# Kernel tuning notes

Measured on AMD Instinct MI355X. Metric: run time of the kernel, lower is better.

## Reference

```python
import jax, jax.numpy as jnp
import numpy as np

NUM_HEADS = 8
NUM_GROUPS = 32
EPS = 1e-5


def setup_inputs() -> dict:
    key = jax.random.key(0)
    ks = jax.random.split(key, 12)
    B, C, H, W = 8, 512, 32, 32
    E = 512
    s = 1.0 / np.sqrt(C)
    inp = {
        "input_tensor": jax.random.normal(ks[0], (B, C, H, W), dtype=jnp.float32),
        "Wq": jax.random.normal(ks[1], (C, E), dtype=jnp.float32) * s,
        "bq": jnp.zeros((E,), dtype=jnp.float32),
        "Wk": jax.random.normal(ks[2], (C, E), dtype=jnp.float32) * s,
        "bk": jnp.zeros((E,), dtype=jnp.float32),
        "Wv": jax.random.normal(ks[3], (C, E), dtype=jnp.float32) * s,
        "bv": jnp.zeros((E,), dtype=jnp.float32),
        "Wo": jax.random.normal(ks[4], (E, E), dtype=jnp.float32) * s,
        "bo": jnp.zeros((E,), dtype=jnp.float32),
        "gamma": jnp.ones((E,), dtype=jnp.float32),
        "beta": jnp.zeros((E,), dtype=jnp.float32),
    }
    return inp


def reference(input_tensor, Wq, bq, Wk, bk, Wv, bv, Wo, bo, gamma, beta):
    B, C, H, W = input_tensor.shape
    E = Wq.shape[1]
    nH = NUM_HEADS
    hd = E // nH
    S = H * W

    # [B, C, H, W] -> [B, S, C]
    x = input_tensor.reshape(B, C, S).transpose(0, 2, 1)

    q = (x @ Wq + bq).reshape(B, S, nH, hd).transpose(0, 2, 1, 3)  # [B, h, S, d]
    k = (x @ Wk + bk).reshape(B, S, nH, hd).transpose(0, 2, 1, 3)
    v = (x @ Wv + bv).reshape(B, S, nH, hd).transpose(0, 2, 1, 3)

    scale = hd ** (-0.5)
    scores = jnp.einsum("bhqd,bhkd->bhqk", q, k) * scale
    weights = jax.nn.softmax(scores, axis=-1)
    attn = jnp.einsum("bhqk,bhkd->bhqd", weights, v)  # [B, h, S, d]

    attn = attn.transpose(0, 2, 1, 3).reshape(B, S, E)
    out = attn @ Wo + bo  # [B, S, E]
    out = out.transpose(0, 2, 1).reshape(B, E, H, W)

    y = out + input_tensor

    # GroupNorm over (channels_per_group, H, W)
    G = NUM_GROUPS
    yg = y.reshape(B, G, E // G, H, W)
    mean = jnp.mean(yg, axis=(2, 3, 4), keepdims=True)
    var = jnp.var(yg, axis=(2, 3, 4), keepdims=True)
    yn = ((yg - mean) * jax.lax.rsqrt(var + EPS)).reshape(B, E, H, W)
    return yn * gamma[None, :, None, None] + beta[None, :, None, None]
```

## Files before the change

kernel.cpp:

```cpp
#include <hip/hip_runtime.h>
#include <math.h>

constexpr int Bn  = 8;
constexpr int Cc  = 512;
constexpr int Ss  = 1024;
constexpr int Ee  = 512;
constexpr int nHd = 8;
constexpr int Hd  = 64;
constexpr int Gg  = 32;
constexpr int Cpg = 16;

typedef __bf16 bf16x8 __attribute__((ext_vector_type(8)));
typedef float  f32x4  __attribute__((ext_vector_type(4)));
typedef float  f32x16 __attribute__((ext_vector_type(16)));
typedef unsigned u32x4 __attribute__((ext_vector_type(4)));

__device__ inline __bf16 cvt_bf16(float f) {
    unsigned u = __builtin_bit_cast(unsigned, f);
    u += 0x7fffu + ((u >> 16) & 1u);
    unsigned short h = (unsigned short)(u >> 16);
    return __builtin_bit_cast(__bf16, h);
}

__device__ inline void gld16(const __bf16* g, __bf16* l) {
    __builtin_amdgcn_global_load_lds(
        (const __attribute__((address_space(1))) void*)g,
        (__attribute__((address_space(3))) void*)l, 16, 0, 0);
}

__device__ inline unsigned pk_bf16_rtz(float hi, float lo) {
    return __builtin_amdgcn_perm(__builtin_bit_cast(unsigned, hi),
                                 __builtin_bit_cast(unsigned, lo), 0x07060302u);
}

__global__ __launch_bounds__(256) void transpose_xw(
    const float* __restrict__ x, __bf16* __restrict__ xt,
    const float* __restrict__ w0, const float* __restrict__ w1,
    const float* __restrict__ w2, const float* __restrict__ w3,
    __bf16* __restrict__ d0, __bf16* __restrict__ d1,
    __bf16* __restrict__ d2, __bf16* __restrict__ d3,
    float* __restrict__ stats)
{
    __shared__ float T[32][33];
    const int r8 = threadIdx.x >> 5, c32 = threadIdx.x & 31;
    const int z = blockIdx.z;
    if (z < 8) {
        const int b = z, c0 = blockIdx.y * 32, s0 = blockIdx.x * 32;
#pragma unroll
        for (int i = 0; i < 4; i++)
            T[r8 + i * 8][c32] =
                x[((size_t)b * Cc + c0 + r8 + i * 8) * Ss + s0 + c32];
        __syncthreads();
#pragma unroll
        for (int i = 0; i < 4; i++)
            xt[((size_t)b * Ss + s0 + r8 + i * 8) * Cc + c0 + c32] =
                cvt_bf16(T[c32][r8 + i * 8]);
    } else {
        if (z == 8 && blockIdx.x == 0 && blockIdx.y == 0) {
            stats[threadIdx.x] = 0.0f;
            stats[threadIdx.x + 256] = 0.0f;
        }
        if (blockIdx.x >= 16) return;
        const int m = z - 8;
        const float* src = (m == 0) ? w0 : (m == 1) ? w1 : (m == 2) ? w2 : w3;
        __bf16* dst = (m == 0) ? d0 : (m == 1) ? d1 : (m == 2) ? d2 : d3;
        const int e0 = blockIdx.x * 32, c0 = blockIdx.y * 32;
#pragma unroll
        for (int i = 0; i < 4; i++)
            T[r8 + i * 8][c32] = src[(size_t)(c0 + r8 + i * 8) * Ee + e0 + c32];
        __syncthreads();
#pragma unroll
        for (int i = 0; i < 4; i++)
            dst[(size_t)(e0 + r8 + i * 8) * Cc + c0 + c32] =
                cvt_bf16(T[c32][r8 + i * 8]);
    }
}

__global__ __launch_bounds__(256) void qkv_mfma(
    const __bf16* __restrict__ xt,
    const __bf16* __restrict__ wqt, const __bf16* __restrict__ wkt,
    const __bf16* __restrict__ wvt,
    const float* __restrict__ bq, const float* __restrict__ bk,
    const float* __restrict__ bv,
    __bf16* __restrict__ qb, __bf16* __restrict__ kb, __bf16* __restrict__ vt)
{
    const int b = blockIdx.z;
    const int wsel = blockIdx.y >> 2;
    const int e0 = (blockIdx.y & 3) * 128;
    const int s0 = blockIdx.x * 128;
    const __bf16* A  = xt + (size_t)b * Ss * Cc;
    const __bf16* Bm = (wsel == 0) ? wqt : (wsel == 1) ? wkt : wvt;
    const float*  bias = (wsel == 0) ? bq : (wsel == 1) ? bk : bv;

    __shared__ __align__(16) char smem[128 * 136 * 2];
    __bf16* As = (__bf16*)smem;
    __bf16* Bs = (__bf16*)(smem + 8192);
    __bf16* T  = (__bf16*)smem;

    const int wave = threadIdx.x >> 6, lane = threadIdx.x & 63;
    const int lid = lane & 15, quad = lane >> 4;
    const int wm = wave & 1, wn = wave >> 1;
    const int srow = lane >> 2, sch = lane & 3;

    f32x4 acc[4][4] = {};

    for (int k0 = 0; k0 < Cc; k0 += 32) {
#pragma unroll
        for (int i = 0; i < 2; i++) {
            const int inst = wave * 2 + i;
            const int r = inst * 16 + srow;
            gld16(&A [(size_t)(s0 + r) * Cc + k0 + sch * 8], &As[inst * 512]);
            gld16(&Bm[(size_t)(e0 + r) * Cc + k0 + sch * 8], &Bs[inst * 512]);
        }
        __syncthreads();
        bf16x8 af[4], bf[4];
#pragma unroll
        for (int i = 0; i < 4; i++)
            af[i] = *(const bf16x8*)&As[(wm * 64 + i * 16 + lid) * 32 + quad * 8];
#pragma unroll
        for (int j = 0; j < 4; j++)
            bf[j] = *(const bf16x8*)&Bs[(wn * 64 + j * 16 + lid) * 32 + quad * 8];
#pragma unroll
        for (int i = 0; i < 4; i++)
#pragma unroll
            for (int j = 0; j < 4; j++)
                acc[i][j] = __builtin_amdgcn_mfma_f32_16x16x32_bf16(
                    af[i], bf[j], acc[i][j], 0, 0, 0);
        __syncthreads();
    }

    float bj[4];
#pragma unroll
    for (int j = 0; j < 4; j++) bj[j] = bias[e0 + wn * 64 + j * 16 + lid];

    if (wsel == 2) {
#pragma unroll
        for (int i = 0; i < 4; i++) {
            const int s4 = wm * 64 + i * 16 + quad * 4;
#pragma unroll
            for (int j = 0; j < 4; j++) {
                const int e_l = wn * 64 + j * 16 + lid;
                unsigned short u0 = __builtin_bit_cast(unsigned short, cvt_bf16(acc[i][j][0] + bj[j]));
                unsigned short u1 = __builtin_bit_cast(unsigned short, cvt_bf16(acc[i][j][1] + bj[j]));
                unsigned short u2 = __builtin_bit_cast(unsigned short, cvt_bf16(acc[i][j][2] + bj[j]));
                unsigned short u3 = __builtin_bit_cast(unsigned short, cvt_bf16(acc[i][j][3] + bj[j]));
                uint2 pk;
                pk.x = (unsigned)u0 | ((unsigned)u1 << 16);
                pk.y = (unsigned)u2 | ((unsigned)u3 << 16);
                *(uint2*)&T[e_l * 136 + s4] = pk;
            }
        }
        __syncthreads();
        const int t = threadIdx.x;
#pragma unroll
        for (int it = 0; it < 8; it++) {
            const int idx = t + it * 256;
            const int e_l = idx >> 4, c8 = (idx & 15) * 8;
            bf16x8 val = *(const bf16x8*)&T[e_l * 136 + c8];
            const int e_g = e0 + e_l;
            const int head = e_g >> 6, d = e_g & 63;
            *(bf16x8*)&vt[(((size_t)b * nHd + head) * Hd + d) * Ss + s0 + c8] = val;
        }
    } else {
        __bf16* outp = (wsel == 0) ? qb : kb;
#pragma unroll
        for (int i = 0; i < 4; i++) {
#pragma unroll
            for (int j = 0; j < 4; j++) {
                const int e1 = e0 + wn * 64 + j * 16 + lid;
                const int head = e1 >> 6, d = e1 & 63;
#pragma unroll
                for (int r = 0; r < 4; r++) {
                    const int s1 = s0 + wm * 64 + i * 16 + quad * 4 + r;
                    outp[(((size_t)b * nHd + head) * Ss + s1) * Hd + d] =
                        cvt_bf16(acc[i][j][r] + bj[j]);
                }
            }
        }
    }
}

__global__ __launch_bounds__(256, 2) void attn_mfma(
    const __bf16* __restrict__ q, const __bf16* __restrict__ k,
    const __bf16* __restrict__ vt, __bf16* __restrict__ attn_out)
{
    const int bh = blockIdx.x;
    const int s0 = blockIdx.y * 128;
    const __bf16* qp = q  + (size_t)bh * Ss * Hd;
    const __bf16* kp = k  + (size_t)bh * Ss * Hd;
    const __bf16* vp = vt + (size_t)bh * Hd * Ss;

    __shared__ __align__(16) __bf16 Ks[128 * 64];
    __shared__ __align__(16) __bf16 Vs[64 * 128];

    const int wave = threadIdx.x >> 6, lane = threadIdx.x & 63;
    const int nl = lane & 31, h = lane >> 5;

    const int sq = s0 + wave * 32 + nl;
    bf16x8 qf[4];
#pragma unroll
    for (int kk2 = 0; kk2 < 4; kk2++)
        qf[kk2] = *(const bf16x8*)&qp[(size_t)sq * Hd + kk2 * 16 + h * 8];

    f32x16 oacc[2] = {};
    float rs = 0.0f;
    const float cexp = 0.125f * 1.44269504f;

    const int srow8 = lane >> 3, sch8 = lane & 7;
    const int srow4 = lane >> 4, sch16 = lane & 15;

    for (int kt = 0; kt < 8; kt++) {
#pragma unroll
        for (int i = 0; i < 4; i++) {
            const int inst = wave * 4 + i;
            const int rK = inst * 8 + srow8;
            gld16(&kp[(size_t)(kt * 128 + rK) * Hd + ((sch8 ^ (rK & 7)) * 8)],
                  &Ks[inst * 512]);
            const int dR = inst * 4 + srow4;
            gld16(&vp[(size_t)dR * Ss + kt * 128 + ((sch16 ^ (dR & 15)) * 8)],
                  &Vs[inst * 512]);
        }
        __syncthreads();

        f32x16 sc[4] = {};
#pragma unroll
        for (int kk2 = 0; kk2 < 4; kk2++) {
#pragma unroll
            for (int mt = 0; mt < 4; mt++) {
                bf16x8 kf = *(const bf16x8*)&Ks[(mt * 32 + nl) * 64 +
                                                (((2 * kk2 + h) ^ (nl & 7)) * 8)];
                sc[mt] = __builtin_amdgcn_mfma_f32_32x32x16_bf16(
                    kf, qf[kk2], sc[mt], 0, 0, 0);
            }
        }

        unsigned frag[8][4];
#pragma unroll
        for (int mt = 0; mt < 4; mt++) {
            float p[16];
#pragma unroll
            for (int r = 0; r < 16; r++) {
                p[r] = __builtin_amdgcn_exp2f(sc[mt][r] * cexp);
                rs += p[r];
            }
            unsigned G[4][2];
#pragma unroll
            for (int qg = 0; qg < 4; qg++) {
                G[qg][0] = pk_bf16_rtz(p[4 * qg + 1], p[4 * qg + 0]);
                G[qg][1] = pk_bf16_rtz(p[4 * qg + 3], p[4 * qg + 2]);
            }
            const unsigned sA0 = h ? G[0][0] : G[1][0];
            const unsigned sA1 = h ? G[0][1] : G[1][1];
            const unsigned sB0 = h ? G[2][0] : G[3][0];
            const unsigned sB1 = h ? G[2][1] : G[3][1];
            const unsigned rA0 = __shfl_xor(sA0, 32, 64);
            const unsigned rA1 = __shfl_xor(sA1, 32, 64);
            const unsigned rB0 = __shfl_xor(sB0, 32, 64);
            const unsigned rB1 = __shfl_xor(sB1, 32, 64);
            frag[2 * mt][0]     = h ? rA0     : G[0][0];
            frag[2 * mt][1]     = h ? rA1     : G[0][1];
            frag[2 * mt][2]     = h ? G[1][0] : rA0;
            frag[2 * mt][3]     = h ? G[1][1] : rA1;
            frag[2 * mt + 1][0] = h ? rB0     : G[2][0];
            frag[2 * mt + 1][1] = h ? rB1     : G[2][1];
            frag[2 * mt + 1][2] = h ? G[3][0] : rB0;
            frag[2 * mt + 1][3] = h ? G[3][1] : rB1;
        }

#pragma unroll
        for (int kk = 0; kk < 8; kk++) {
            u32x4 fv = {frag[kk][0], frag[kk][1], frag[kk][2], frag[kk][3]};
            bf16x8 pf = __builtin_bit_cast(bf16x8, fv);
#pragma unroll
            for (int dt = 0; dt < 2; dt++) {
                bf16x8 vf = *(const bf16x8*)&Vs[(dt * 32 + nl) * 128 +
                                                (((kk * 2 + h) ^ (nl & 15)) * 8)];
                oacc[dt] = __builtin_amdgcn_mfma_f32_32x32x16_bf16(
                    pf, vf, oacc[dt], 0, 0, 0);
            }
        }
        __syncthreads();
    }

    rs += __shfl_xor(rs, 32, 64);
    const float inv = 1.0f / rs;
    const int b = bh >> 3, head = bh & 7;
#pragma unroll
    for (int r = 0; r < 16; r++) {
        const int rowq = (r & 3) + 8 * (r >> 2) + 4 * h;
        const float invr = __shfl(inv, rowq, 64);
        const int s1 = s0 + wave * 32 + rowq;
#pragma unroll
        for (int dt = 0; dt < 2; dt++)
            attn_out[((size_t)b * Ss + s1) * Ee + head * Hd + dt * 32 + nl] =
                cvt_bf16(oacc[dt][r] * invr);
    }
}

__global__ __launch_bounds__(256) void outproj_mfma(
    const __bf16* __restrict__ attnb, const __bf16* __restrict__ wot,
    const float* __restrict__ bo, const float* __restrict__ xin,
    __bf16* __restrict__ y, float* __restrict__ stats)
{
    const int b  = blockIdx.z;
    const int e0 = blockIdx.y * 128;
    const int s0 = blockIdx.x * 128;
    const __bf16* Bm = attnb + (size_t)b * Ss * Ee;

    __shared__ __align__(16) __bf16 As[128 * 32];
    __shared__ __align__(16) __bf16 Bs[128 * 32];

    const int wave = threadIdx.x >> 6, lane = threadIdx.x & 63;
    const int lid = lane & 15, quad = lane >> 4;
    const int wm = wave & 1, wn = wave >> 1;
    const int srow = lane >> 2, sch = lane & 3;

    f32x4 acc[4][4] = {};

    for (int k0 = 0; k0 < Ee; k0 += 32) {
#pragma unroll
        for (int i = 0; i < 2; i++) {
            const int inst = wave * 2 + i;
            const int r = inst * 16 + srow;
            gld16(&wot[(size_t)(e0 + r) * Ee + k0 + sch * 8], &As[inst * 512]);
            gld16(&Bm [(size_t)(s0 + r) * Ee + k0 + sch * 8], &Bs[inst * 512]);
        }
        __syncthreads();
        bf16x8 af[4], bf[4];
#pragma unroll
        for (int i = 0; i < 4; i++)
            af[i] = *(const bf16x8*)&As[(wm * 64 + i * 16 + lid) * 32 + quad * 8];
#pragma unroll
        for (int j = 0; j < 4; j++)
            bf[j] = *(const bf16x8*)&Bs[(wn * 64 + j * 16 + lid) * 32 + quad * 8];
#pragma unroll
        for (int i = 0; i < 4; i++)
#pragma unroll
            for (int j = 0; j < 4; j++)
                acc[i][j] = __builtin_amdgcn_mfma_f32_16x16x32_bf16(
                    af[i], bf[j], acc[i][j], 0, 0, 0);
        __syncthreads();
    }

    float gs[4] = {}, gs2[4] = {};
#pragma unroll
    for (int i = 0; i < 4; i++) {
#pragma unroll
        for (int r = 0; r < 4; r++) {
            const int eo1 = e0 + wm * 64 + i * 16 + quad * 4 + r;
            const float bb = bo[eo1];
#pragma unroll
            for (int j = 0; j < 4; j++) {
                const int s1 = s0 + wn * 64 + j * 16 + lid;
                const size_t idx = ((size_t)b * Ee + eo1) * Ss + s1;
                const float v = acc[i][j][r] + bb + xin[idx];
                y[idx] = cvt_bf16(v);
                gs[i]  += v;
                gs2[i] += v * v;
            }
        }
    }
#pragma unroll
    for (int i = 0; i < 4; i++) {
        float a = gs[i], c = gs2[i];
#pragma unroll
        for (int off = 32; off > 0; off >>= 1) {
            a += __shfl_down(a, off, 64);
            c += __shfl_down(c, off, 64);
        }
        if (lane == 0) {
            const int g = (e0 >> 4) + wm * 4 + i;
            atomicAdd(&stats[(b * Gg + g) * 2 + 0], a);
            atomicAdd(&stats[(b * Gg + g) * 2 + 1], c);
        }
    }
}

__global__ __launch_bounds__(256) void gnorm_kernel(
    const __bf16* __restrict__ y, const float* __restrict__ gamma,
    const float* __restrict__ beta, const float* __restrict__ stats,
    float* __restrict__ out)
{
    const int bg = blockIdx.x;
    const int b = bg >> 5, g = bg & 31;
    const size_t base = ((size_t)b * Ee + g * Cpg) * Ss;
    const bf16x8* y8 = (const bf16x8*)(y + base);
    constexpr int N8 = (Cpg * Ss) / 8;
    constexpr float Nf = (float)(Cpg * Ss);

    const float mean = stats[bg * 2 + 0] / Nf;
    const float var  = stats[bg * 2 + 1] / Nf - mean * mean;
    const float rstd = rsqrtf(var + 1e-5f);

    for (int i = threadIdx.x; i < N8; i += 256) {
        bf16x8 vv = y8[i];
        const int c = g * Cpg + (i >> 7);
        const float gm = gamma[c] * rstd;
        const float bt = beta[c];
        f32x4 r0, r1;
#pragma unroll
        for (int j = 0; j < 4; j++) r0[j] = ((float)vv[j] - mean) * gm + bt;
#pragma unroll
        for (int j = 0; j < 4; j++) r1[j] = ((float)vv[4 + j] - mean) * gm + bt;
        *(f32x4*)&out[base + (size_t)i * 8]     = r0;
        *(f32x4*)&out[base + (size_t)i * 8 + 4] = r1;
    }
}

extern "C" void kernel_launch(void* const* d_in, const int* in_sizes, int n_in,
                              void* d_out, int out_size, void* d_ws, size_t ws_size,
                              hipStream_t stream)
{
    const float* x     = (const float*)d_in[0];
    const float* Wq    = (const float*)d_in[1];
    const float* bq    = (const float*)d_in[2];
    const float* Wk    = (const float*)d_in[3];
    const float* bk    = (const float*)d_in[4];
    const float* Wv    = (const float*)d_in[5];
    const float* bv    = (const float*)d_in[6];
    const float* Wo    = (const float*)d_in[7];
    const float* bo    = (const float*)d_in[8];
    const float* gamma = (const float*)d_in[9];
    const float* beta  = (const float*)d_in[10];
    float* out = (float*)d_out;

    char* ws = (char*)d_ws;
    __bf16* xt    = (__bf16*)ws;
    __bf16* wqt   = (__bf16*)(ws + (8u << 20));
    __bf16* wkt   = (__bf16*)(ws + (8u << 20) + (512u << 10));
    __bf16* wvt   = (__bf16*)(ws + (9u << 20));
    __bf16* wot   = (__bf16*)(ws + (9u << 20) + (512u << 10));
    __bf16* qb    = (__bf16*)(ws + (10u << 20));
    __bf16* kb    = (__bf16*)(ws + (18u << 20));
    __bf16* vtb   = (__bf16*)(ws + (26u << 20));
    __bf16* attnb = (__bf16*)(ws + (34u << 20));
    __bf16* yb    = (__bf16*)(ws + (42u << 20));
    float*  statb = (float*) (ws + (50u << 20));

    transpose_xw<<<dim3(32, 16, 12), 256, 0, stream>>>(
        x, xt, Wq, Wk, Wv, Wo, wqt, wkt, wvt, wot, statb);

    qkv_mfma<<<dim3(Ss / 128, 12, Bn), 256, 0, stream>>>(
        xt, wqt, wkt, wvt, bq, bk, bv, qb, kb, vtb);

    attn_mfma<<<dim3(Bn * nHd, Ss / 128), 256, 0, stream>>>(qb, kb, vtb, attnb);

    outproj_mfma<<<dim3(Ss / 128, Ee / 128, Bn), 256, 0, stream>>>(
        attnb, wot, bo, x, yb, statb);

    gnorm_kernel<<<Bn * Gg, 256, 0, stream>>>(yb, gamma, beta, statb, out);
}
```

Before: 164.1 us.

## Double-buffer LDS tiles in QKV, attention and out-projection kernels

```diff
diff --git a/kernel.cpp b/kernel.cpp
--- a/kernel.cpp
+++ b/kernel.cpp
@@ -93,9 +93,7 @@
     const float*  bias = (wsel == 0) ? bq : (wsel == 1) ? bk : bv;
 
     __shared__ __align__(16) char smem[128 * 136 * 2];
-    __bf16* As = (__bf16*)smem;
-    __bf16* Bs = (__bf16*)(smem + 8192);
-    __bf16* T  = (__bf16*)smem;
+    __bf16* T = (__bf16*)smem;
 
     const int wave = threadIdx.x >> 6, lane = threadIdx.x & 63;
     const int lid = lane & 15, quad = lane >> 4;
@@ -104,30 +102,39 @@
 
     f32x4 acc[4][4] = {};
 
-    for (int k0 = 0; k0 < Cc; k0 += 32) {
+    auto stage = [&](int k0, int bufi) {
+        __bf16* Asb = (__bf16*)(smem + bufi * 16384);
+        __bf16* Bsb = (__bf16*)(smem + bufi * 16384 + 8192);
 #pragma unroll
         for (int i = 0; i < 2; i++) {
             const int inst = wave * 2 + i;
             const int r = inst * 16 + srow;
-            gld16(&A [(size_t)(s0 + r) * Cc + k0 + sch * 8], &As[inst * 512]);
-            gld16(&Bm[(size_t)(e0 + r) * Cc + k0 + sch * 8], &Bs[inst * 512]);
-        }
-        __syncthreads();
+            gld16(&A [(size_t)(s0 + r) * Cc + k0 + sch * 8], &Asb[inst * 512]);
+            gld16(&Bm[(size_t)(e0 + r) * Cc + k0 + sch * 8], &Bsb[inst * 512]);
+        }
+    };
+
+    stage(0, 0);
+    for (int it = 0; it < 16; it++) {
+        __syncthreads();
+        if (it + 1 < 16) stage((it + 1) * 32, (it + 1) & 1);
+        const __bf16* Asb = (const __bf16*)(smem + (it & 1) * 16384);
+        const __bf16* Bsb = Asb + 4096;
         bf16x8 af[4], bf[4];
 #pragma unroll
         for (int i = 0; i < 4; i++)
-            af[i] = *(const bf16x8*)&As[(wm * 64 + i * 16 + lid) * 32 + quad * 8];
+            af[i] = *(const bf16x8*)&Asb[(wm * 64 + i * 16 + lid) * 32 + quad * 8];
 #pragma unroll
         for (int j = 0; j < 4; j++)
-            bf[j] = *(const bf16x8*)&Bs[(wn * 64 + j * 16 + lid) * 32 + quad * 8];
+            bf[j] = *(const bf16x8*)&Bsb[(wn * 64 + j * 16 + lid) * 32 + quad * 8];
 #pragma unroll
         for (int i = 0; i < 4; i++)
 #pragma unroll
             for (int j = 0; j < 4; j++)
                 acc[i][j] = __builtin_amdgcn_mfma_f32_16x16x32_bf16(
                     af[i], bf[j], acc[i][j], 0, 0, 0);
-        __syncthreads();
-    }
+    }
+    __syncthreads();
 
     float bj[4];
 #pragma unroll
@@ -190,8 +197,8 @@
     const __bf16* kp = k  + (size_t)bh * Ss * Hd;
     const __bf16* vp = vt + (size_t)bh * Hd * Ss;
 
-    __shared__ __align__(16) __bf16 Ks[128 * 64];
-    __shared__ __align__(16) __bf16 Vs[64 * 128];
+    __shared__ __align__(16) __bf16 Ks[2][128 * 64];
+    __shared__ __align__(16) __bf16 Vs[2][64 * 128];
 
     const int wave = threadIdx.x >> 6, lane = threadIdx.x & 63;
     const int nl = lane & 31, h = lane >> 5;
@@ -209,26 +216,35 @@
     const int srow8 = lane >> 3, sch8 = lane & 7;
     const int srow4 = lane >> 4, sch16 = lane & 15;
 
-    for (int kt = 0; kt < 8; kt++) {
+    auto stageKV = [&](int kt, int bufi) {
+        __bf16* Ksb = Ks[bufi];
+        __bf16* Vsb = Vs[bufi];
 #pragma unroll
         for (int i = 0; i < 4; i++) {
             const int inst = wave * 4 + i;
             const int rK = inst * 8 + srow8;
             gld16(&kp[(size_t)(kt * 128 + rK) * Hd + ((sch8 ^ (rK & 7)) * 8)],
-                  &Ks[inst * 512]);
+                  &Ksb[inst * 512]);
             const int dR = inst * 4 + srow4;
             gld16(&vp[(size_t)dR * Ss + kt * 128 + ((sch16 ^ (dR & 15)) * 8)],
-                  &Vs[inst * 512]);
-        }
-        __syncthreads();
+                  &Vsb[inst * 512]);
+        }
+    };
+
+    stageKV(0, 0);
+    for (int kt = 0; kt < 8; kt++) {
+        __syncthreads();
+        if (kt + 1 < 8) stageKV(kt + 1, (kt + 1) & 1);
+        const __bf16* Ksb = Ks[kt & 1];
+        const __bf16* Vsb = Vs[kt & 1];
 
         f32x16 sc[4] = {};
 #pragma unroll
         for (int kk2 = 0; kk2 < 4; kk2++) {
 #pragma unroll
             for (int mt = 0; mt < 4; mt++) {
-                bf16x8 kf = *(const bf16x8*)&Ks[(mt * 32 + nl) * 64 +
-                                                (((2 * kk2 + h) ^ (nl & 7)) * 8)];
+                bf16x8 kf = *(const bf16x8*)&Ksb[(mt * 32 + nl) * 64 +
+                                                 (((2 * kk2 + h) ^ (nl & 7)) * 8)];
                 sc[mt] = __builtin_amdgcn_mfma_f32_32x32x16_bf16(
                     kf, qf[kk2], sc[mt], 0, 0, 0);
             }
@@ -273,13 +289,12 @@
             bf16x8 pf = __builtin_bit_cast(bf16x8, fv);
 #pragma unroll
             for (int dt = 0; dt < 2; dt++) {
-                bf16x8 vf = *(const bf16x8*)&Vs[(dt * 32 + nl) * 128 +
-                                                (((kk * 2 + h) ^ (nl & 15)) * 8)];
+                bf16x8 vf = *(const bf16x8*)&Vsb[(dt * 32 + nl) * 128 +
+                                                 (((kk * 2 + h) ^ (nl & 15)) * 8)];
                 oacc[dt] = __builtin_amdgcn_mfma_f32_32x32x16_bf16(
                     pf, vf, oacc[dt], 0, 0, 0);
             }
         }
-        __syncthreads();
     }
 
     rs += __shfl_xor(rs, 32, 64);
@@ -307,8 +322,7 @@
     const int s0 = blockIdx.x * 128;
     const __bf16* Bm = attnb + (size_t)b * Ss * Ee;
 
-    __shared__ __align__(16) __bf16 As[128 * 32];
-    __shared__ __align__(16) __bf16 Bs[128 * 32];
+    __shared__ __align__(16) char smem[32768];
 
     const int wave = threadIdx.x >> 6, lane = threadIdx.x & 63;
     const int lid = lane & 15, quad = lane >> 4;
@@ -317,29 +331,37 @@
 
     f32x4 acc[4][4] = {};
 
-    for (int k0 = 0; k0 < Ee; k0 += 32) {
+    auto stage = [&](int k0, int bufi) {
+        __bf16* Asb = (__bf16*)(smem + bufi * 16384);
+        __bf16* Bsb = (__bf16*)(smem + bufi * 16384 + 8192);
 #pragma unroll
         for (int i = 0; i < 2; i++) {
             const int inst = wave * 2 + i;
             const int r = inst * 16 + srow;
-            gld16(&wot[(size_t)(e0 + r) * Ee + k0 + sch * 8], &As[inst * 512]);
-            gld16(&Bm [(size_t)(s0 + r) * Ee + k0 + sch * 8], &Bs[inst * 512]);
-        }
-        __syncthreads();
+            gld16(&wot[(size_t)(e0 + r) * Ee + k0 + sch * 8], &Asb[inst * 512]);
+            gld16(&Bm [(size_t)(s0 + r) * Ee + k0 + sch * 8], &Bsb[inst * 512]);
+        }
+    };
+
+    stage(0, 0);
+    for (int it = 0; it < 16; it++) {
+        __syncthreads();
+        if (it + 1 < 16) stage((it + 1) * 32, (it + 1) & 1);
+        const __bf16* Asb = (const __bf16*)(smem + (it & 1) * 16384);
+        const __bf16* Bsb = Asb + 4096;
         bf16x8 af[4], bf[4];
 #pragma unroll
         for (int i = 0; i < 4; i++)
-            af[i] = *(const bf16x8*)&As[(wm * 64 + i * 16 + lid) * 32 + quad * 8];
+            af[i] = *(const bf16x8*)&Asb[(wm * 64 + i * 16 + lid) * 32 + quad * 8];
 #pragma unroll
         for (int j = 0; j < 4; j++)
-            bf[j] = *(const bf16x8*)&Bs[(wn * 64 + j * 16 + lid) * 32 + quad * 8];
+            bf[j] = *(const bf16x8*)&Bsb[(wn * 64 + j * 16 + lid) * 32 + quad * 8];
 #pragma unroll
         for (int i = 0; i < 4; i++)
 #pragma unroll
             for (int j = 0; j < 4; j++)
                 acc[i][j] = __builtin_amdgcn_mfma_f32_16x16x32_bf16(
                     af[i], bf[j], acc[i][j], 0, 0, 0);
-        __syncthreads();
     }
 
     float gs[4] = {}, gs2[4] = {};
```

Measured after the change: 155.9 us (median of 2 runs). 1.05x faster.
